# Optimization experiments

Hardware: AMD Instinct MI355X
Metric: run time of the kernel (lower is better)

The kernel has to match this reference:

```python
import jax, jax.numpy as jnp
import numpy as np

T = 22        # TypeEncoder.tensor_size() (assumed)
H = 2         # attention heads
C = 64        # hc_graph (per-head out channels)
L = 3         # num_hops
LEAFCAT = 5   # len(LeafType.valid_categories()) (assumed)
NSIZES = 8    # len(LeafType.valid_sizes()) (assumed)
HL = 64       # hc_linear
HT = 64       # hc_task == hc_leafsize
SLOPE = 0.2   # PyG GATConv negative_slope


def _gat(x, src, dst, W, asrc, adst, b):
    # PyG GATConv (concat=True, dropout=0, self-loops already appended to src/dst)
    N = x.shape[0]
    h = (x @ W).reshape(N, H, C)                      # [N,H,C]
    a_s = jnp.einsum('nhc,hc->nh', h, asrc)            # per-node src score
    a_d = jnp.einsum('nhc,hc->nh', h, adst)            # per-node dst score
    e = jax.nn.leaky_relu(a_s[src] + a_d[dst], SLOPE)  # [E+N,H]
    m = jax.ops.segment_max(e, dst, num_segments=N)
    p = jnp.exp(e - m[dst])
    s = jax.ops.segment_sum(p, dst, num_segments=N)
    alpha = p / (s[dst] + 1e-16)                       # scatter-softmax over in-edges
    out = jax.ops.segment_sum(h[src] * alpha[:, :, None], dst, num_segments=N)
    return out.reshape(N, H * C) + b


def _mlp2(z, W1, b1, W2, b2):
    return jax.nn.relu(z @ W1 + b1) @ W2 + b2


def setup_inputs() -> dict:
    key = jax.random.key(0)
    ks = jax.random.split(key, 32)
    N, E, NG, NPG = 102400, 1228800, 256, 400
    D = H * C
    g = lambda k, shp, fan: (jax.random.normal(k, shp, jnp.float32) / np.sqrt(fan)).astype(jnp.float32)
    z = lambda *shp: jnp.zeros(shp, jnp.float32)
    return {
        'x': jax.random.normal(ks[0], (N, D), jnp.float32),
        'edge_index': jax.random.randint(ks[1], (2, E), 0, N),
        'batch': jnp.repeat(jnp.arange(NG, dtype=jnp.int32), NPG),
        'gat_W': g(ks[2], (L, D, D), D),
        'gat_asrc': g(ks[3], (L, H, C), C),
        'gat_adst': g(ks[4], (L, H, C), C),
        'gat_b': z(L, D),
        'shared_W': g(ks[5], (D + T, HL), D + T),
        'shared_b': z(HL),
        'ptr_W1': g(ks[6], (3, HL, HT), HL), 'ptr_b1': z(3, HT),
        'ptr_W2': g(ks[7], (3, HT, 3), HT), 'ptr_b2': z(3, 3),
        'cat_W1': g(ks[8], (HL, HT), HL), 'cat_b1': z(HT),
        'cat_W2': g(ks[9], (HT, LEAFCAT), HT), 'cat_b2': z(LEAFCAT),
        'sf_W1': g(ks[10], (2, HL, HT), HL), 'sf_b1': z(2, HT),
        'sf_W2': g(ks[11], (2, HT, 1), HT), 'sf_b2': z(2, 1),
        'bool_W1': g(ks[12], (HL + T + LEAFCAT + 2, HT), HL + T + LEAFCAT + 2), 'bool_b1': z(HT),
        'bool_W2': g(ks[13], (HT, 1), HT), 'bool_b2': z(1),
        'size_W1': g(ks[14], (HL + T + LEAFCAT + 3, HT), HL + T + LEAFCAT + 3), 'size_b1': z(HT),
        'size_W2': g(ks[15], (HT, NSIZES), HT), 'size_b2': z(NSIZES),
    }


def reference(x, edge_index, batch, gat_W, gat_asrc, gat_adst, gat_b,
              shared_W, shared_b, ptr_W1, ptr_b1, ptr_W2, ptr_b2,
              cat_W1, cat_b1, cat_W2, cat_b2, sf_W1, sf_b1, sf_W2, sf_b2,
              bool_W1, bool_b1, bool_W2, bool_b2, size_W1, size_b1, size_W2, size_b2):
    N = x.shape[0]
    num_graphs = int(batch[-1]) + 1                    # batch is sorted per-graph ids
    node0 = jnp.searchsorted(batch, jnp.arange(num_graphs))  # first node of each graph
    dtype_vec = x[node0, :T]                           # NodeEncoder.split_node_vec dtype slice
    loops = jnp.arange(N)
    src = jnp.concatenate([edge_index[0], loops])      # GATConv add_self_loops=True
    dst = jnp.concatenate([edge_index[1], loops])
    h = x
    for l in range(L):
        h = _gat(h, src, dst, gat_W[l], gat_asrc[l], gat_adst[l], gat_b[l])
        if l < L - 1:
            h = jax.nn.relu(h)
    zf = jax.nn.relu(jnp.concatenate([h[node0], dtype_vec], axis=1) @ shared_W + shared_b)
    # 3 pointer heads, batched
    p = jax.nn.relu(jnp.einsum('gh,khd->kgd', zf, ptr_W1) + ptr_b1[:, None, :])
    ptr = jnp.einsum('kgd,kdo->kgo', p, ptr_W2) + ptr_b2[:, None, :]
    cat_logits = _mlp2(zf, cat_W1, cat_b1, cat_W2, cat_b2)
    q = jax.nn.relu(jnp.einsum('gh,khd->kgd', zf, sf_W1) + sf_b1[:, None, :])
    sf = jnp.einsum('kgd,kdo->kgo', q, sf_W2) + sf_b2[:, None, :]
    signed, floating = sf[0], sf[1]
    bool_in = jnp.concatenate([zf, dtype_vec, cat_logits, signed, floating], axis=1)
    bool_logit = _mlp2(bool_in, bool_W1, bool_b1, bool_W2, bool_b2)
    size_in = jnp.concatenate([bool_in, bool_logit], axis=1)
    size_logits = _mlp2(size_in, size_W1, size_b1, size_W2, size_b2)
    return (ptr[0], ptr[1], ptr[2], cat_logits, signed, floating, bool_logit, size_logits)
```

## Files before the change

kernel.cpp:

```cpp
#include <hip/hip_runtime.h>
#include <hip/hip_bf16.h>

typedef __hip_bfloat16 bf16;
typedef __attribute__((ext_vector_type(8))) short short8;
typedef __attribute__((ext_vector_type(4))) float floatx4;

#define MF(a, b, c) __builtin_amdgcn_mfma_f32_16x16x32_bf16(a, b, c, 0, 0, 0)

__device__ __forceinline__ float b2f(bf16 v) { return __bfloat162float(v); }
__device__ __forceinline__ unsigned short f2us(float f) {
    bf16 h = __float2bfloat16(f);
    return *(unsigned short*)&h;
}
__device__ __forceinline__ float lo2f(unsigned hv) { return __uint_as_float(hv << 16); }
__device__ __forceinline__ float hi2f(unsigned hv) { return __uint_as_float(hv & 0xffff0000u); }
__device__ __forceinline__ float leaky(float v) { return v > 0.f ? v : 0.2f * v; }

__device__ __forceinline__ float ldw(const void* p, size_t i, int f32) {
    return f32 ? ((const float*)p)[i] : b2f(((const bf16*)p)[i]);
}

template <int F32>
__device__ __forceinline__ float LDWt(const void* p, size_t i) {
    return F32 ? ((const float*)p)[i] : b2f(((const bf16*)p)[i]);
}

__device__ __forceinline__ int or16(const int* f) {
    int r = 0;
#pragma unroll
    for (int j = 0; j < 16; j++) r |= f[j];
    return r;
}

__device__ __forceinline__ void quadred(float part[4]) {
#pragma unroll
    for (int m = 1; m <= 8; m <<= 1)
#pragma unroll
        for (int r = 0; r < 4; r++) part[r] += __shfl_xor(part[r], m);
}

__global__ void k_detect_zero(const void* x, int* flagv, char* zbase, size_t zbytes,
                              const int* __restrict__ batch, int* __restrict__ node0,
                              unsigned char* __restrict__ rootb,
                              unsigned char* __restrict__ flag2, int N, int zBlocks) {
    int b = blockIdx.x;
    int t = threadIdx.x;
    if (b < 16) {
        __shared__ int sbad;
        if (t == 0) sbad = 0;
        __syncthreads();
        float v = b2f(((const bf16*)x)[b * 256 + t]);
        if (!(fabsf(v) < 1e10f)) sbad = 1;
        __syncthreads();
        if (t == 0) flagv[b] = sbad;
    } else if (b < 16 + zBlocks) {
        size_t off = (size_t)(b - 16) * 4096 + (size_t)t * 16;
        if (off < zbytes) *(uint4*)(zbase + off) = make_uint4(0u, 0u, 0u, 0u);
    } else {
        int i = (b - 16 - zBlocks) * 256 + t;
        if (i < N) {
            int bb = batch[i];
            int isroot = (i == 0) || (batch[i - 1] != bb);
            rootb[i] = (unsigned char)isroot;
            flag2[i] = (unsigned char)isroot;
            if (isroot) node0[bb] = i;
        }
    }
}

__global__ void k_prep_fused(const void* __restrict__ x, unsigned short* __restrict__ Ab,
                             int nvec,
                             const void* __restrict__ gw, unsigned short* __restrict__ Wt,
                             const void* as_, const void* ad_, const void* b_,
                             float* asF, float* adF, float* bF,
                             const void* sW_, const void* pW1_, const void* cW1_,
                             const void* fW1_, const void* bW1_, const void* zW1_,
                             unsigned short* __restrict__ Whd,
                             const int* __restrict__ ei, const unsigned char* __restrict__ rootb,
                             unsigned char* __restrict__ flag2, int E,
                             const int* __restrict__ flagv, int nbx8) {
    int b = blockIdx.x;
    int t = threadIdx.x;
    int f32 = or16(flagv);
    if (b < nbx8) {
        if (!f32) return;
        int i = b * 256 + t;
        if (i < nvec) {
            float4 a = ((const float4*)x)[2 * i];
            float4 c = ((const float4*)x)[2 * i + 1];
            uint4 o;
            o.x = ((unsigned)f2us(a.y) << 16) | f2us(a.x);
            o.y = ((unsigned)f2us(a.w) << 16) | f2us(a.z);
            o.z = ((unsigned)f2us(c.y) << 16) | f2us(c.x);
            o.w = ((unsigned)f2us(c.w) << 16) | f2us(c.z);
            ((uint4*)Ab)[i] = o;
        }
    } else if (b < nbx8 + 192) {
        int i = (b - nbx8) * 256 + t;
        int l = i >> 14, rem = i & 16383, n = rem >> 7, k = rem & 127;
        Wt[i] = f2us(ldw(gw, (size_t)l * 16384 + (size_t)k * 128 + n, f32));
    } else if (b < nbx8 + 194) {
        int i = (b - nbx8 - 192) * 256 + t;
        if (i < 384) {
            asF[i] = ldw(as_, i, f32);
            adF[i] = ldw(ad_, i, f32);
            bF[i] = ldw(b_, i, f32);
        }
    } else if (b < nbx8 + 194 + 184) {
        int i = (b - nbx8 - 194) * 256 + t;
        float v;
        if (i < 10240) {
            int n = i / 160, k = i - n * 160;
            v = (k < 150) ? ldw(sW_, (size_t)k * 64 + n, f32) : 0.f;
        } else if (i < 22528) {
            int j = i - 10240;
            int kk = j >> 12, r = j & 4095, n = r >> 6, k = r & 63;
            v = ldw(pW1_, (size_t)kk * 4096 + (size_t)k * 64 + n, f32);
        } else if (i < 26624) {
            int j = i - 22528;
            int n = j >> 6, k = j & 63;
            v = ldw(cW1_, (size_t)k * 64 + n, f32);
        } else if (i < 34816) {
            int j = i - 26624;
            int kk = j >> 12, r = j & 4095, n = r >> 6, k = r & 63;
            v = ldw(fW1_, (size_t)kk * 4096 + (size_t)k * 64 + n, f32);
        } else if (i < 40960) {
            int j = i - 34816;
            int n = j / 96, k = j - n * 96;
            v = (k < 93) ? ldw(bW1_, (size_t)k * 64 + n, f32) : 0.f;
        } else {
            int j = i - 40960;
            int n = j / 96, k = j - n * 96;
            v = (k < 94) ? ldw(zW1_, (size_t)k * 64 + n, f32) : 0.f;
        }
        Whd[i] = f2us(v);
    } else {
        int e = (b - nbx8 - 194 - 184) * 256 + t;
        if (e < E && rootb[ei[E + e]]) flag2[ei[e]] = 1;
    }
}

__global__ void k_hist_masked(const int* __restrict__ ei, const unsigned char* __restrict__ flag1,
                              int* __restrict__ counts, int E) {
    int e = blockIdx.x * blockDim.x + threadIdx.x;
    if (e < E) {
        int d = ei[E + e];
        if (flag1[d]) atomicAdd(&counts[d], 1);
    }
}

__global__ void k_scan3x(const int* __restrict__ counts,
                         const unsigned char* __restrict__ flag1,
                         const unsigned char* __restrict__ flag2,
                         int* __restrict__ offs, int* __restrict__ wp1, int* __restrict__ wp2,
                         int* __restrict__ bsums, int n) {
    __shared__ int s[256];
    int tid = threadIdx.x;
    int i = blockIdx.x * 256 + tid;
#pragma unroll
    for (int a = 0; a < 3; a++) {
        int v = 0;
        if (i < n) v = (a == 0) ? counts[i] : (a == 1) ? (int)flag1[i] : (int)flag2[i];
        s[tid] = v;
        __syncthreads();
        for (int d = 1; d < 256; d <<= 1) {
            int t2 = (tid >= d) ? s[tid - d] : 0;
            __syncthreads();
            s[tid] += t2;
            __syncthreads();
        }
        int incl = s[tid];
        if (i < n) {
            if (a == 0) offs[i] = incl - v;
            else if (a == 1) wp1[i] = incl - v;
            else wp2[i] = incl - v;
        }
        if (tid == 255) bsums[a * 512 + blockIdx.x] = incl;
        __syncthreads();
    }
}

__global__ void k_scan2x(int* __restrict__ bsums, int nb, int* __restrict__ nact) {
    __shared__ int s[512];
    int tid = threadIdx.x;
#pragma unroll
    for (int a = 0; a < 3; a++) {
        int* arr = bsums + a * 512;
        int v = (tid < nb) ? arr[tid] : 0;
        s[tid] = v;
        __syncthreads();
        for (int d = 1; d < 512; d <<= 1) {
            int t2 = (tid >= d) ? s[tid - d] : 0;
            __syncthreads();
            s[tid] += t2;
            __syncthreads();
        }
        arr[tid] = s[tid] - v;
        if (a >= 1 && tid == 511) nact[a - 1] = s[511];
        __syncthreads();
    }
}

__global__ void k_scatter_wl(const int* __restrict__ ei, const int* __restrict__ offs,
                             const int* __restrict__ bsums, int* __restrict__ cur,
                             const unsigned char* __restrict__ flag1,
                             const unsigned char* __restrict__ flag2,
                             const int* __restrict__ wp1, const int* __restrict__ wp2,
                             int* __restrict__ adj, int* __restrict__ wl1, int* __restrict__ wl2,
                             int E, int N, int eBlocks) {
    int b = blockIdx.x;
    if (b < eBlocks) {
        int e = b * 256 + threadIdx.x;
        if (e >= E) return;
        int d = ei[E + e];
        if (!flag1[d]) return;
        int r = atomicAdd(&cur[d], 1);
        adj[offs[d] + bsums[d >> 8] + r] = ei[e];
    } else {
        int i = (b - eBlocks) * 256 + threadIdx.x;
        if (i < N) {
            if (flag1[i]) wl1[wp1[i] + bsums[512 + (i >> 8)]] = i;
            if (flag2[i]) wl2[wp2[i] + bsums[1024 + (i >> 8)]] = i;
        }
    }
}

__device__ __forceinline__ void gemm_body(
    const unsigned short* __restrict__ Asrc, const unsigned short* __restrict__ Wt,
    unsigned short* __restrict__ Bb, float4* __restrict__ asadv,
    const float* __restrict__ asF, const float* __restrict__ adF, int N,
    const int* __restrict__ wl, const int* __restrict__ nactp, int bb) {
    __shared__ __align__(16) unsigned short Ws[128 * 136];
    __shared__ __align__(16) unsigned short Cs[64 * 136];

    int t = threadIdx.x;
    int r0 = bb * 64;
    int nact = wl ? *nactp : N;
    if (r0 >= nact) return;

    {
        const uint4* src = (const uint4*)Wt;
#pragma unroll
        for (int k = 0; k < 8; k++) {
            int j = t + k * 256;
            int row = j >> 4, c16 = j & 15;
            *(uint4*)&Ws[row * 136 + c16 * 8] = src[j];
        }
    }
    __syncthreads();

    int lane = t & 63;
    int w = t >> 6;
    int ln = lane & 15;
    int quad = lane >> 4;

    int idx = r0 + w * 16 + ln;
    bool valid = idx < nact;
    int arow = idx < N ? idx : N - 1;
    if (wl) arow = valid ? wl[idx] : 0;
    bool wave_active = __any((int)valid);

    if (wave_active) {
        const unsigned short* ap = Asrc + (size_t)arow * 128 + quad * 8;

        short8 afrag[4];
        if (valid) {
#pragma unroll
            for (int kt = 0; kt < 4; kt++)
                afrag[kt] = *(const short8*)(ap + kt * 32);
        } else {
#pragma unroll
            for (int kt = 0; kt < 4; kt++)
                afrag[kt] = (short8){0, 0, 0, 0, 0, 0, 0, 0};
        }

        floatx4 acc[8];
#pragma unroll
        for (int nt = 0; nt < 8; nt++) acc[nt] = (floatx4){0.f, 0.f, 0.f, 0.f};

#pragma unroll
        for (int nt = 0; nt < 8; nt++) {
            const unsigned short* wp = Ws + (nt * 16 + ln) * 136 + quad * 8;
#pragma unroll
            for (int kt = 0; kt < 4; kt++) {
                short8 bfrag = *(const short8*)(wp + kt * 32);
                acc[nt] = MF(afrag[kt], bfrag, acc[nt]);
            }
        }

        float as0[4] = {0, 0, 0, 0}, as1[4] = {0, 0, 0, 0};
        float ad0[4] = {0, 0, 0, 0}, ad1[4] = {0, 0, 0, 0};
#pragma unroll
        for (int nt = 0; nt < 8; nt++) {
            float asc = asF[nt * 16 + ln];
            float adc = adF[nt * 16 + ln];
#pragma unroll
            for (int r = 0; r < 4; r++) {
                float v = acc[nt][r];
                Cs[(w * 16 + quad * 4 + r) * 136 + nt * 16 + ln] = f2us(v);
                if (nt < 4) { as0[r] += v * asc; ad0[r] += v * adc; }
                else        { as1[r] += v * asc; ad1[r] += v * adc; }
            }
        }
#pragma unroll
        for (int mask = 1; mask <= 8; mask <<= 1) {
#pragma unroll
            for (int r = 0; r < 4; r++) {
                as0[r] += __shfl_xor(as0[r], mask);
                as1[r] += __shfl_xor(as1[r], mask);
                ad0[r] += __shfl_xor(ad0[r], mask);
                ad1[r] += __shfl_xor(ad1[r], mask);
            }
        }
        if (ln == 0) {
#pragma unroll
            for (int r = 0; r < 4; r++) {
                int idx3 = r0 + w * 16 + quad * 4 + r;
                if (idx3 < nact) {
                    int row = wl ? wl[idx3] : idx3;
                    asadv[row] = make_float4(as0[r], as1[r], ad0[r], ad1[r]);
                }
            }
        }
    }
    __syncthreads();

    {
        int idx2 = r0 + (t >> 2);
        int cseg = (t & 3) * 32;
        if (idx2 < nact) {
            int grow = wl ? wl[idx2] : idx2;
            const short8* srcp = (const short8*)&Cs[(t >> 2) * 136 + cseg];
            short8* dstp = (short8*)&Bb[(size_t)grow * 128 + cseg];
#pragma unroll
            for (int u = 0; u < 4; u++) dstp[u] = srcp[u];
        }
    }
}

__global__ __launch_bounds__(256) void k_gemm_mfma(
    const unsigned short* __restrict__ Ab, const unsigned short* __restrict__ Wt,
    unsigned short* __restrict__ Bb, float4* __restrict__ asadv,
    const float* __restrict__ asF, const float* __restrict__ adF, int N,
    const int* __restrict__ wl, const int* __restrict__ nactp) {
    gemm_body(Ab, Wt, Bb, asadv, asF, adF, N, wl, nactp, blockIdx.x);
}

__global__ __launch_bounds__(256) void k_gemm0_mark(
    const unsigned short* __restrict__ Ab, const void* __restrict__ xraw,
    const unsigned short* __restrict__ Wt,
    unsigned short* __restrict__ Bb, float4* __restrict__ asadv,
    const float* __restrict__ asF, const float* __restrict__ adF, int N,
    const int* __restrict__ ei, const unsigned char* __restrict__ flag2,
    unsigned char* __restrict__ flag1, int E, int markE, int markN,
    const int* __restrict__ flagv) {
    int b = blockIdx.x;
    if (b < markE) {
        int e = b * 256 + threadIdx.x;
        if (e < E && flag2[ei[E + e]]) flag1[ei[e]] = 1;
        return;
    }
    if (b < markE + markN) {
        int i = (b - markE) * 256 + threadIdx.x;
        if (i < N && flag2[i]) flag1[i] = 1;
        return;
    }
    const unsigned short* Asrc = or16(flagv) ? Ab : (const unsigned short*)xraw;
    gemm_body(Asrc, Wt, Bb, asadv, asF, adF, N, nullptr, nullptr, b - markE - markN);
}

__global__ void k_gat_agg(const uint2* __restrict__ Bu2, const float4* __restrict__ asadv,
                          const int* __restrict__ offs, const int* __restrict__ bsums,
                          const int* __restrict__ counts,
                          const int* __restrict__ adj, const float* __restrict__ biasF,
                          uint2* __restrict__ Au2, float2* __restrict__ pE,
                          const int* __restrict__ nactp, int nfix, int dorelu, int byidx,
                          const int* __restrict__ wl) {
    int wave = (blockIdx.x * blockDim.x + threadIdx.x) >> 6;
    int lane = threadIdx.x & 63;
    int hl = lane & 31;
    int hb = lane & 32;
    int idx = wave * 2 + (lane >> 5);
    int n = nfix ? nfix : *nactp;
    if (idx >= n) return;
    int node = wl[idx];
    int head = hl >> 4;

    float4 self = asadv[node];
    float ad0 = self.z, ad1 = self.w;
    float es0 = __expf(leaky(self.x + ad0));
    float es1 = __expf(leaky(self.y + ad1));

    int o = offs[node] + bsums[node >> 8];
    int c = counts[node];
    uint2 hvs = Bu2[(size_t)node * 32 + hl];
    float acc0, acc1, acc2, acc3;

    if (c <= 32) {
        int src_r = 0;
        float p0 = 0.f, p1 = 0.f;
        if (hl < c) {
            src_r = adj[o + hl];
            float4 av = asadv[src_r];
            p0 = __expf(leaky(av.x + ad0));
            p1 = __expf(leaky(av.y + ad1));
        }
        float t0 = p0, t1 = p1;
#pragma unroll
        for (int mask = 1; mask <= 16; mask <<= 1) {
            t0 += __shfl_xor(t0, mask);
            t1 += __shfl_xor(t1, mask);
        }
        float inv0 = 1.f / (es0 + t0 + 1e-16f);
        float inv1 = 1.f / (es1 + t1 + 1e-16f);
        p0 *= inv0;
        p1 *= inv1;
        float aself = head ? es1 * inv1 : es0 * inv0;
        acc0 = aself * lo2f(hvs.x);
        acc1 = aself * hi2f(hvs.x);
        acc2 = aself * lo2f(hvs.y);
        acc3 = aself * hi2f(hvs.y);

        uint2 hq[4];
#pragma unroll
        for (int j = 0; j < 4; j++) {
            int s2 = __shfl(src_r, hb + j);
            hq[j] = make_uint2(0u, 0u);
            if (j < c) hq[j] = Bu2[(size_t)s2 * 32 + hl];
        }

        for (int base = 0; base < c; base += 4) {
            uint2 cu[4];
            float av4[4];
#pragma unroll
            for (int j = 0; j < 4; j++) {
                cu[j] = hq[j];
                int idx2 = (base + j) & 31;
                float a0 = __shfl(p0, hb + idx2);
                float a1 = __shfl(p1, hb + idx2);
                float a = head ? a1 : a0;
                av4[j] = (base + j < c) ? a : 0.f;
            }
#pragma unroll
            for (int j = 0; j < 4; j++) {
                int nx = base + 4 + j;
                int s2 = __shfl(src_r, hb + (nx & 31));
                if (nx < c) hq[j] = Bu2[(size_t)s2 * 32 + hl];
            }
#pragma unroll
            for (int j = 0; j < 4; j++) {
                acc0 += av4[j] * lo2f(cu[j].x);
                acc1 += av4[j] * hi2f(cu[j].x);
                acc2 += av4[j] * lo2f(cu[j].y);
                acc3 += av4[j] * hi2f(cu[j].y);
            }
        }
    } else {
        float sum0 = es0, sum1 = es1;
        for (int base = 0; base < c; base += 32) {
            int i = base + hl;
            float p0 = 0.f, p1 = 0.f;
            if (i < c) {
                int s = adj[o + i];
                float4 av = asadv[s];
                p0 = __expf(leaky(av.x + ad0));
                p1 = __expf(leaky(av.y + ad1));
                pE[o + i] = make_float2(p0, p1);
            }
            float t0 = p0, t1 = p1;
#pragma unroll
            for (int mask = 1; mask <= 16; mask <<= 1) {
                t0 += __shfl_xor(t0, mask);
                t1 += __shfl_xor(t1, mask);
            }
            sum0 += t0; sum1 += t1;
        }
        float inv0 = 1.f / (sum0 + 1e-16f);
        float inv1 = 1.f / (sum1 + 1e-16f);
        float aself = head ? es1 * inv1 : es0 * inv0;
        float invh = head ? inv1 : inv0;
        acc0 = aself * lo2f(hvs.x);
        acc1 = aself * hi2f(hvs.x);
        acc2 = aself * lo2f(hvs.y);
        acc3 = aself * hi2f(hvs.y);
        for (int i = 0; i < c; i++) {
            int s = adj[o + i];
            float2 pp = pE[o + i];
            uint2 hv = Bu2[(size_t)s * 32 + hl];
            float a = (head ? pp.y : pp.x) * invh;
            acc0 += a * lo2f(hv.x);
            acc1 += a * hi2f(hv.x);
            acc2 += a * lo2f(hv.y);
            acc3 += a * hi2f(hv.y);
        }
    }

    float4 bb4 = ((const float4*)biasF)[hl];
    float q0 = acc0 + bb4.x;
    float q1 = acc1 + bb4.y;
    float q2 = acc2 + bb4.z;
    float q3 = acc3 + bb4.w;
    if (dorelu) {
        q0 = fmaxf(q0, 0.f); q1 = fmaxf(q1, 0.f);
        q2 = fmaxf(q2, 0.f); q3 = fmaxf(q3, 0.f);
    }
    Au2[(size_t)(byidx ? idx : node) * 32 + hl] =
        make_uint2(((unsigned)f2us(q1) << 16) | f2us(q0),
                   ((unsigned)f2us(q3) << 16) | f2us(q2));
}

template <int F32>
__device__ void heads_mfma_body(
    const unsigned* __restrict__ hroot32, const void* __restrict__ x,
    const int* __restrict__ node0, const unsigned short* __restrict__ Whd,
    const void* sb, const void* pb1, const void* pW2, const void* pb2,
    const void* cb1, const void* cW2, const void* cb2,
    const void* fb1, const void* fW2, const void* fb2,
    const void* bb1, const void* bW2, const void* bb2,
    const void* zb1, const void* zW2, const void* zb2,
    void* __restrict__ outv) {
    __shared__ __align__(16) unsigned short hinS[64 * 168];
    __shared__ __align__(16) unsigned short TwS[4][16 * 168];

    int t = threadIdx.x;
    int g0b = blockIdx.x * 64;
    bf16* outb = (bf16*)outv;
    float* outf = (float*)outv;
#define STORE(idx, val) do { if (F32) outf[idx] = (val); else outb[idx] = __float2bfloat16(val); } while (0)

    {
        unsigned* h32 = (unsigned*)hinS;
        for (int j = t; j < 64 * 64; j += 256) {
            int gl = j >> 6, c = j & 63;
            h32[gl * 84 + c] = hroot32[(size_t)(g0b + gl) * 64 + c];
        }
        for (int j = t; j < 64 * 20; j += 256) {
            int gl = j / 20, c = j - gl * 20;
            int n0 = node0[g0b + gl];
            int k0 = 2 * c;
            float d0 = (k0 < 22) ? LDWt<F32>(x, (size_t)n0 * 128 + k0) : 0.f;
            float d1 = (k0 + 1 < 22) ? LDWt<F32>(x, (size_t)n0 * 128 + k0 + 1) : 0.f;
            h32[gl * 84 + 64 + c] = ((unsigned)f2us(d1) << 16) | f2us(d0);
        }
    }
    __syncthreads();

    int w = t >> 6;
    int lane = t & 63;
    int ln = lane & 15, quad = lane >> 4;
    unsigned short* T = TwS[w];
    int gq = quad * 4;
    int gw0 = g0b + w * 16;

    for (int j = lane; j < 16 * 32; j += 64) {
        int gl = j >> 5, c = j & 31;
        T[gl * 168 + 64 + c] =
            (c < 22) ? hinS[(w * 16 + gl) * 168 + 128 + c] : (unsigned short)0;
    }

    short8 afA[5];
#pragma unroll
    for (int kt = 0; kt < 5; kt++)
        afA[kt] = *(const short8*)&hinS[(w * 16 + ln) * 168 + quad * 8 + kt * 32];
#pragma unroll
    for (int nt = 0; nt < 4; nt++) {
        floatx4 acc = (floatx4){0.f, 0.f, 0.f, 0.f};
        const unsigned short* bp = Whd + (nt * 16 + ln) * 160 + quad * 8;
#pragma unroll
        for (int kt = 0; kt < 5; kt++)
            acc = MF(afA[kt], *(const short8*)(bp + kt * 32), acc);
        float bias = LDWt<F32>(sb, nt * 16 + ln);
#pragma unroll
        for (int r = 0; r < 4; r++)
            T[(gq + r) * 168 + nt * 16 + ln] = f2us(fmaxf(acc[r] + bias, 0.f));
    }
    __syncthreads();

    short8 af20 = *(const short8*)&T[ln * 168 + quad * 8];
    short8 af21 = *(const short8*)&T[ln * 168 + quad * 8 + 32];

#pragma unroll
    for (int k = 0; k < 3; k++) {
        const unsigned short* Bw = Whd + 10240 + k * 4096;
        floatx4 acc[4];
#pragma unroll
        for (int nt = 0; nt < 4; nt++) {
            floatx4 a = (floatx4){0.f, 0.f, 0.f, 0.f};
            const unsigned short* bp = Bw + (nt * 16 + ln) * 64 + quad * 8;
            a = MF(af20, *(const short8*)bp, a);
            a = MF(af21, *(const short8*)(bp + 32), a);
            float b1 = LDWt<F32>(pb1, k * 64 + nt * 16 + ln);
#pragma unroll
            for (int r = 0; r < 4; r++) a[r] = fmaxf(a[r] + b1, 0.f);
            acc[nt] = a;
        }
#pragma unroll
        for (int o = 0; o < 3; o++) {
            float w2[4], part[4];
#pragma unroll
            for (int nt = 0; nt < 4; nt++)
                w2[nt] = LDWt<F32>(pW2, (size_t)k * 192 + (size_t)(nt * 16 + ln) * 3 + o);
#pragma unroll
            for (int r = 0; r < 4; r++)
                part[r] = acc[0][r] * w2[0] + acc[1][r] * w2[1] +
                          acc[2][r] * w2[2] + acc[3][r] * w2[3];
            quadred(part);
            if (ln == 0) {
                float b2 = LDWt<F32>(pb2, k * 3 + o);
#pragma unroll
                for (int r = 0; r < 4; r++)
                    STORE(k * 768 + (gw0 + gq + r) * 3 + o, part[r] + b2);
            }
        }
    }

    {
        const unsigned short* Bw = Whd + 22528;
        floatx4 acc[4];
#pragma unroll
        for (int nt = 0; nt < 4; nt++) {
            floatx4 a = (floatx4){0.f, 0.f, 0.f, 0.f};
            const unsigned short* bp = Bw + (nt * 16 + ln) * 64 + quad * 8;
            a = MF(af20, *(const short8*)bp, a);
            a = MF(af21, *(const short8*)(bp + 32), a);
            float b1 = LDWt<F32>(cb1, nt * 16 + ln);
#pragma unroll
            for (int r = 0; r < 4; r++) a[r] = fmaxf(a[r] + b1, 0.f);
            acc[nt] = a;
        }
#pragma unroll
        for (int o = 0; o < 5; o++) {
            float w2[4], part[4];
#pragma unroll
            for (int nt = 0; nt < 4; nt++)
                w2[nt] = LDWt<F32>(cW2, (size_t)(nt * 16 + ln) * 5 + o);
#pragma unroll
            for (int r = 0; r < 4; r++)
                part[r] = acc[0][r] * w2[0] + acc[1][r] * w2[1] +
                          acc[2][r] * w2[2] + acc[3][r] * w2[3];
            quadred(part);
            if (ln == 0) {
                float b2 = LDWt<F32>(cb2, o);
#pragma unroll
                for (int r = 0; r < 4; r++) {
                    float v = part[r] + b2;
                    T[(gq + r) * 168 + 86 + o] = f2us(v);
                    STORE(2304 + (gw0 + gq + r) * 5 + o, v);
                }
            }
        }
    }

#pragma unroll
    for (int k = 0; k < 2; k++) {
        const unsigned short* Bw = Whd + 26624 + k * 4096;
        floatx4 acc[4];
#pragma unroll
        for (int nt = 0; nt < 4; nt++) {
            floatx4 a = (floatx4){0.f, 0.f, 0.f, 0.f};
            const unsigned short* bp = Bw + (nt * 16 + ln) * 64 + quad * 8;
            a = MF(af20, *(const short8*)bp, a);
            a = MF(af21, *(const short8*)(bp + 32), a);
            float b1 = LDWt<F32>(fb1, k * 64 + nt * 16 + ln);
#pragma unroll
            for (int r = 0; r < 4; r++) a[r] = fmaxf(a[r] + b1, 0.f);
            acc[nt] = a;
        }
        float w2[4], part[4];
#pragma unroll
        for (int nt = 0; nt < 4; nt++)
            w2[nt] = LDWt<F32>(fW2, (size_t)k * 64 + nt * 16 + ln);
#pragma unroll
        for (int r = 0; r < 4; r++)
            part[r] = acc[0][r] * w2[0] + acc[1][r] * w2[1] +
                      acc[2][r] * w2[2] + acc[3][r] * w2[3];
        quadred(part);
        if (ln == 0) {
            float b2 = LDWt<F32>(fb2, k);
#pragma unroll
            for (int r = 0; r < 4; r++) {
                float v = part[r] + b2;
                T[(gq + r) * 168 + 91 + k] = f2us(v);
                STORE(3584 + k * 256 + (gw0 + gq + r), v);
            }
        }
    }
    __syncthreads();

    short8 af3 = *(const short8*)&T[ln * 168 + 64 + quad * 8];

    {
        const unsigned short* Bw = Whd + 34816;
        floatx4 acc[4];
#pragma unroll
        for (int nt = 0; nt < 4; nt++) {
            floatx4 a = (floatx4){0.f, 0.f, 0.f, 0.f};
            const unsigned short* bp = Bw + (nt * 16 + ln) * 96 + quad * 8;
            a = MF(af20, *(const short8*)bp, a);
            a = MF(af21, *(const short8*)(bp + 32), a);
            a = MF(af3, *(const short8*)(bp + 64), a);
            float b1 = LDWt<F32>(bb1, nt * 16 + ln);
#pragma unroll
            for (int r = 0; r < 4; r++) a[r] = fmaxf(a[r] + b1, 0.f);
            acc[nt] = a;
        }
        float w2[4], part[4];
#pragma unroll
        for (int nt = 0; nt < 4; nt++)
            w2[nt] = LDWt<F32>(bW2, nt * 16 + ln);
#pragma unroll
        for (int r = 0; r < 4; r++)
            part[r] = acc[0][r] * w2[0] + acc[1][r] * w2[1] +
                      acc[2][r] * w2[2] + acc[3][r] * w2[3];
        quadred(part);
        if (ln == 0) {
            float b2 = LDWt<F32>(bb2, 0);
#pragma unroll
            for (int r = 0; r < 4; r++) {
                float v = part[r] + b2;
                T[(gq + r) * 168 + 93] = f2us(v);
                STORE(4096 + (gw0 + gq + r), v);
            }
        }
    }
    __syncthreads();

    af3 = *(const short8*)&T[ln * 168 + 64 + quad * 8];

    {
        const unsigned short* Bw = Whd + 40960;
        floatx4 acc[4];
#pragma unroll
        for (int nt = 0; nt < 4; nt++) {
            floatx4 a = (floatx4){0.f, 0.f, 0.f, 0.f};
            const unsigned short* bp = Bw + (nt * 16 + ln) * 96 + quad * 8;
            a = MF(af20, *(const short8*)bp, a);
            a = MF(af21, *(const short8*)(bp + 32), a);
            a = MF(af3, *(const short8*)(bp + 64), a);
            float b1 = LDWt<F32>(zb1, nt * 16 + ln);
#pragma unroll
            for (int r = 0; r < 4; r++) a[r] = fmaxf(a[r] + b1, 0.f);
            acc[nt] = a;
        }
#pragma unroll
        for (int o = 0; o < 8; o++) {
            float w2[4], part[4];
#pragma unroll
            for (int nt = 0; nt < 4; nt++)
                w2[nt] = LDWt<F32>(zW2, (size_t)(nt * 16 + ln) * 8 + o);
#pragma unroll
            for (int r = 0; r < 4; r++)
                part[r] = acc[0][r] * w2[0] + acc[1][r] * w2[1] +
                          acc[2][r] * w2[2] + acc[3][r] * w2[3];
            quadred(part);
            if (ln == 0) {
                float b2 = LDWt<F32>(zb2, o);
#pragma unroll
                for (int r = 0; r < 4; r++)
                    STORE(4352 + (gw0 + gq + r) * 8 + o, part[r] + b2);
            }
        }
    }
#undef STORE
}

__global__ __launch_bounds__(256) void k_heads_mfma(
    const unsigned* __restrict__ hroot32, const void* __restrict__ x,
    const int* __restrict__ node0, const unsigned short* __restrict__ Whd,
    const void* sb, const void* pb1, const void* pW2, const void* pb2,
    const void* cb1, const void* cW2, const void* cb2,
    const void* fb1, const void* fW2, const void* fb2,
    const void* bb1, const void* bW2, const void* bb2,
    const void* zb1, const void* zW2, const void* zb2,
    void* __restrict__ outv, const int* __restrict__ flagv) {
    if (or16(flagv))
        heads_mfma_body<1>(hroot32, x, node0, Whd, sb, pb1, pW2, pb2, cb1, cW2, cb2,
                           fb1, fW2, fb2, bb1, bW2, bb2, zb1, zW2, zb2, outv);
    else
        heads_mfma_body<0>(hroot32, x, node0, Whd, sb, pb1, pW2, pb2, cb1, cW2, cb2,
                           fb1, fW2, fb2, bb1, bW2, bb2, zb1, zW2, zb2, outv);
}


extern "C" void kernel_launch(void* const* d_in, const int* in_sizes, int n_in,
                              void* d_out, int out_size, void* d_ws, size_t ws_size,
                              hipStream_t stream) {
    const void* x     = d_in[0];
    const int*  ei    = (const int*)d_in[1];
    const int*  batch = (const int*)d_in[2];

    int N = in_sizes[0] / 128;
    int E = in_sizes[1] / 2;

    char* w = (char*)d_ws;
    float4* asad = (float4*)w;              w += (size_t)N * 16;
    unsigned short* A = (unsigned short*)w; w += (size_t)N * 128 * 2;
    unsigned short* B = (unsigned short*)w; w += (size_t)N * 128 * 2;
    float2* pE = (float2*)w;                w += (size_t)E * 8;
    unsigned short* Wt = (unsigned short*)w; w += 3 * 16384 * 2;
    unsigned short* Whd = (unsigned short*)w; w += 47104 * 2;
    float* asF = (float*)w;                 w += 384 * 4;
    float* adF = (float*)w;                 w += 384 * 4;
    float* bF = (float*)w;                  w += 384 * 4;
    int* offs = (int*)w;                    w += (size_t)N * 4;
    int* wp1 = (int*)w;                     w += (size_t)N * 4;
    int* wp2 = (int*)w;                     w += (size_t)N * 4;
    int* wl1 = (int*)w;                     w += (size_t)N * 4;
    int* wl2 = (int*)w;                     w += (size_t)N * 4;
    int* adj = (int*)w;                     w += (size_t)E * 4;
    int* bsums = (int*)w;                   w += 3 * 512 * 4;
    int* node0 = (int*)w;                   w += 256 * 4;
    int* nact = (int*)w;                    w += 64;
    unsigned* hroot = (unsigned*)w;         w += 256 * 128 * 2;
    char* zbase = w;
    int* counts = (int*)w;                  w += (size_t)N * 4;
    int* cur = (int*)w;                     w += (size_t)N * 4;
    unsigned char* flag1 = (unsigned char*)w; w += (size_t)N;
    size_t zbytes = (size_t)N * 9;
    int* flagv = (int*)w;                   w += 64;
    unsigned char* rootb = (unsigned char*)w; w += (size_t)N;
    unsigned char* flag2 = (unsigned char*)w; w += (size_t)N;

    int nb = (N + 255) / 256;
    int nvec = N * 16;
    int nbx8 = (nvec + 255) / 256;
    int nbE = (E + 255) / 256;
    int gemmBlocks = (N + 63) / 64;
    int zBlocks = (int)((zbytes + 4095) / 4096);

    k_detect_zero<<<16 + zBlocks + nb, 256, 0, stream>>>(
        x, flagv, zbase, zbytes, batch, node0, rootb, flag2, N, zBlocks);

    k_prep_fused<<<nbx8 + 194 + 184 + nbE, 256, 0, stream>>>(
        x, A, nvec, d_in[3], Wt, d_in[4], d_in[5], d_in[6],
        asF, adF, bF,
        d_in[7], d_in[9], d_in[13], d_in[17], d_in[21], d_in[25], Whd,
        ei, rootb, flag2, E, flagv, nbx8);

    k_gemm0_mark<<<nbE + nb + gemmBlocks, 256, 0, stream>>>(
        A, x, Wt, B, asad, asF, adF, N, ei, flag2, flag1, E, nbE, nb, flagv);

    k_hist_masked<<<nbE, 256, 0, stream>>>(ei, flag1, counts, E);
    k_scan3x<<<nb, 256, 0, stream>>>(counts, flag1, flag2, offs, wp1, wp2, bsums, N);
    k_scan2x<<<1, 512, 0, stream>>>(bsums, nb, nact);
    k_scatter_wl<<<nbE + nb, 256, 0, stream>>>(
        ei, offs, bsums, cur, flag1, flag2, wp1, wp2, adj, wl1, wl2, E, N, nbE);

    int nwaves = (N + 1) / 2;
    int aggblocks = (nwaves + 3) / 4;

    k_gat_agg<<<aggblocks, 256, 0, stream>>>(
        (const uint2*)B, asad, offs, bsums, counts, adj, bF, (uint2*)A, pE,
        nact, 0, 1, 0, wl1);

    k_gemm_mfma<<<gemmBlocks, 256, 0, stream>>>(
        A, Wt + 16384, B, asad, asF + 128, adF + 128, N, wl1, nact);
    k_gat_agg<<<aggblocks, 256, 0, stream>>>(
        (const uint2*)B, asad, offs, bsums, counts, adj, bF + 128, (uint2*)A, pE,
        nact + 1, 0, 1, 0, wl2);

    k_gemm_mfma<<<gemmBlocks, 256, 0, stream>>>(
        A, Wt + 2 * 16384, B, asad, asF + 256, adF + 256, N, wl2, nact + 1);

    k_gat_agg<<<32, 256, 0, stream>>>(
        (const uint2*)B, asad, offs, bsums, counts, adj, bF + 256, (uint2*)hroot, pE,
        nact, 256, 0, 1, node0);

    k_heads_mfma<<<4, 256, 0, stream>>>(
        hroot, x, node0, Whd,
        d_in[8], d_in[10], d_in[11], d_in[12],
        d_in[14], d_in[15], d_in[16],
        d_in[18], d_in[19], d_in[20],
        d_in[22], d_in[23], d_in[24],
        d_in[26], d_in[27], d_in[28],
        d_out, flagv);
}
```

Baseline: 316.3 us.

## Replace CSR adjacency with fixed-slot buckets and drop the count/scan passes

Incoming edges are now scattered into a fixed per-node array of 128 slots, with an overflow list for larger degrees. This removes the histogram kernel, the count scan and the offset computation. The two remaining flag scans and the block-sum scan are merged into one kernel that uses a last-block-done atomic. The GEMM and aggregation kernels become grid-stride loops with smaller fixed grids, and the root-flag/dtype-detect setup is simplified. The cost is a much larger adjacency buffer (N*128 ints) with scattered memory access, plus a linear scan of the overflow list for any node above 128 in-edges.

```diff
diff --git a/kernel.cpp b/kernel.cpp
--- a/kernel.cpp
+++ b/kernel.cpp
@@ -6,6 +6,7 @@
 typedef __attribute__((ext_vector_type(4))) float floatx4;
 
 #define MF(a, b, c) __builtin_amdgcn_mfma_f32_16x16x32_bf16(a, b, c, 0, 0, 0)
+#define ADJ_SLOTS 128
 
 __device__ __forceinline__ float b2f(bf16 v) { return __bfloat162float(v); }
 __device__ __forceinline__ unsigned short f2us(float f) {
@@ -25,13 +26,6 @@
     return F32 ? ((const float*)p)[i] : b2f(((const bf16*)p)[i]);
 }
 
-__device__ __forceinline__ int or16(const int* f) {
-    int r = 0;
-#pragma unroll
-    for (int j = 0; j < 16; j++) r |= f[j];
-    return r;
-}
-
 __device__ __forceinline__ void quadred(float part[4]) {
 #pragma unroll
     for (int m = 1; m <= 8; m <<= 1)
@@ -39,75 +33,75 @@
         for (int r = 0; r < 4; r++) part[r] += __shfl_xor(part[r], m);
 }
 
-__global__ void k_detect_zero(const void* x, int* flagv, char* zbase, size_t zbytes,
+__global__ void k_detect_zero(const void* x, int* flagd, char* zbase, size_t zbytes,
                               const int* __restrict__ batch, int* __restrict__ node0,
-                              unsigned char* __restrict__ rootb,
                               unsigned char* __restrict__ flag2, int N, int zBlocks) {
     int b = blockIdx.x;
     int t = threadIdx.x;
-    if (b < 16) {
+    if (b == 0) {
         __shared__ int sbad;
         if (t == 0) sbad = 0;
         __syncthreads();
-        float v = b2f(((const bf16*)x)[b * 256 + t]);
-        if (!(fabsf(v) < 1e10f)) sbad = 1;
+        const bf16* xb = (const bf16*)x;
+        int bad = 0;
+#pragma unroll
+        for (int j = 0; j < 16; j++) {
+            float v = b2f(xb[t * 16 + j]);
+            if (!(fabsf(v) < 1e10f)) bad = 1;
+        }
+        if (bad) sbad = 1;
         __syncthreads();
-        if (t == 0) flagv[b] = sbad;
-    } else if (b < 16 + zBlocks) {
-        size_t off = (size_t)(b - 16) * 4096 + (size_t)t * 16;
+        if (t == 0) flagd[0] = sbad;
+    } else if (b < 1 + zBlocks) {
+        size_t off = (size_t)(b - 1) * 4096 + (size_t)t * 16;
         if (off < zbytes) *(uint4*)(zbase + off) = make_uint4(0u, 0u, 0u, 0u);
     } else {
-        int i = (b - 16 - zBlocks) * 256 + t;
+        int i = (b - 1 - zBlocks) * 256 + t;
         if (i < N) {
             int bb = batch[i];
             int isroot = (i == 0) || (batch[i - 1] != bb);
-            rootb[i] = (unsigned char)isroot;
             flag2[i] = (unsigned char)isroot;
             if (isroot) node0[bb] = i;
         }
     }
 }
 
-__global__ void k_prep_fused(const void* __restrict__ x, unsigned short* __restrict__ Ab,
-                             int nvec,
-                             const void* __restrict__ gw, unsigned short* __restrict__ Wt,
-                             const void* as_, const void* ad_, const void* b_,
-                             float* asF, float* adF, float* bF,
-                             const void* sW_, const void* pW1_, const void* cW1_,
-                             const void* fW1_, const void* bW1_, const void* zW1_,
-                             unsigned short* __restrict__ Whd,
-                             const int* __restrict__ ei, const unsigned char* __restrict__ rootb,
-                             unsigned char* __restrict__ flag2, int E,
-                             const int* __restrict__ flagv, int nbx8) {
+__global__ void k_prep(const void* __restrict__ x, unsigned short* __restrict__ Ab,
+                       int nvec,
+                       const void* __restrict__ gw, unsigned short* __restrict__ Wt,
+                       const void* as_, const void* ad_, const void* b_,
+                       float* asF, float* adF, float* bF,
+                       const void* sW_, const void* pW1_, const void* cW1_,
+                       const void* fW1_, const void* bW1_, const void* zW1_,
+                       unsigned short* __restrict__ Whd,
+                       const int* __restrict__ ei, const int* __restrict__ batch,
+                       unsigned char* __restrict__ flag2, int E,
+                       const int* __restrict__ flagd, int nbE) {
     int b = blockIdx.x;
     int t = threadIdx.x;
-    int f32 = or16(flagv);
-    if (b < nbx8) {
-        if (!f32) return;
+    if (b < nbE) {
+        int e = b * 256 + t;
+        if (e < E) {
+            int d = ei[E + e];
+            if (d == 0 || batch[d] != batch[d - 1]) flag2[ei[e]] = 1;
+        }
+        return;
+    }
+    int f32 = *flagd;
+    b -= nbE;
+    if (b < 192) {
         int i = b * 256 + t;
-        if (i < nvec) {
-            float4 a = ((const float4*)x)[2 * i];
-            float4 c = ((const float4*)x)[2 * i + 1];
-            uint4 o;
-            o.x = ((unsigned)f2us(a.y) << 16) | f2us(a.x);
-            o.y = ((unsigned)f2us(a.w) << 16) | f2us(a.z);
-            o.z = ((unsigned)f2us(c.y) << 16) | f2us(c.x);
-            o.w = ((unsigned)f2us(c.w) << 16) | f2us(c.z);
-            ((uint4*)Ab)[i] = o;
-        }
-    } else if (b < nbx8 + 192) {
-        int i = (b - nbx8) * 256 + t;
         int l = i >> 14, rem = i & 16383, n = rem >> 7, k = rem & 127;
         Wt[i] = f2us(ldw(gw, (size_t)l * 16384 + (size_t)k * 128 + n, f32));
-    } else if (b < nbx8 + 194) {
-        int i = (b - nbx8 - 192) * 256 + t;
+    } else if (b < 194) {
+        int i = (b - 192) * 256 + t;
         if (i < 384) {
             asF[i] = ldw(as_, i, f32);
             adF[i] = ldw(ad_, i, f32);
             bF[i] = ldw(b_, i, f32);
         }
-    } else if (b < nbx8 + 194 + 184) {
-        int i = (b - nbx8 - 194) * 256 + t;
+    } else if (b < 194 + 184) {
+        int i = (b - 194) * 256 + t;
         float v;
         if (i < 10240) {
             int n = i / 160, k = i - n * 160;
@@ -135,32 +129,35 @@
         }
         Whd[i] = f2us(v);
     } else {
-        int e = (b - nbx8 - 194 - 184) * 256 + t;
-        if (e < E && rootb[ei[E + e]]) flag2[ei[e]] = 1;
-    }
-}
-
-__global__ void k_hist_masked(const int* __restrict__ ei, const unsigned char* __restrict__ flag1,
-                              int* __restrict__ counts, int E) {
-    int e = blockIdx.x * blockDim.x + threadIdx.x;
-    if (e < E) {
-        int d = ei[E + e];
-        if (flag1[d]) atomicAdd(&counts[d], 1);
-    }
-}
-
-__global__ void k_scan3x(const int* __restrict__ counts,
-                         const unsigned char* __restrict__ flag1,
-                         const unsigned char* __restrict__ flag2,
-                         int* __restrict__ offs, int* __restrict__ wp1, int* __restrict__ wp2,
-                         int* __restrict__ bsums, int n) {
+        if (!f32) return;
+        int i0 = (b - 194 - 184) * 256 + t;
+        for (int i = i0; i < nvec; i += 256 * 256) {
+            float4 a = ((const float4*)x)[2 * i];
+            float4 c = ((const float4*)x)[2 * i + 1];
+            uint4 o;
+            o.x = ((unsigned)f2us(a.y) << 16) | f2us(a.x);
+            o.y = ((unsigned)f2us(a.w) << 16) | f2us(a.z);
+            o.z = ((unsigned)f2us(c.y) << 16) | f2us(c.x);
+            o.w = ((unsigned)f2us(c.w) << 16) | f2us(c.z);
+            ((uint4*)Ab)[i] = o;
+        }
+    }
+}
+
+__global__ void k_scan2lane(const unsigned char* __restrict__ flag1,
+                            const unsigned char* __restrict__ flag2,
+                            int* __restrict__ wp1, int* __restrict__ wp2,
+                            int* __restrict__ bsums, int* __restrict__ nact,
+                            int* __restrict__ done, int n, int nb) {
     __shared__ int s[256];
+    __shared__ int s2[512];
+    __shared__ int lastFlag;
     int tid = threadIdx.x;
     int i = blockIdx.x * 256 + tid;
 #pragma unroll
-    for (int a = 0; a < 3; a++) {
+    for (int a = 0; a < 2; a++) {
         int v = 0;
-        if (i < n) v = (a == 0) ? counts[i] : (a == 1) ? (int)flag1[i] : (int)flag2[i];
+        if (i < n) v = a == 0 ? (int)flag1[i] : (int)flag2[i];
         s[tid] = v;
         __syncthreads();
         for (int d = 1; d < 256; d <<= 1) {
@@ -171,42 +168,50 @@
         }
         int incl = s[tid];
         if (i < n) {
-            if (a == 0) offs[i] = incl - v;
-            else if (a == 1) wp1[i] = incl - v;
+            if (a == 0) wp1[i] = incl - v;
             else wp2[i] = incl - v;
         }
         if (tid == 255) bsums[a * 512 + blockIdx.x] = incl;
         __syncthreads();
     }
-}
-
-__global__ void k_scan2x(int* __restrict__ bsums, int nb, int* __restrict__ nact) {
-    __shared__ int s[512];
-    int tid = threadIdx.x;
-#pragma unroll
-    for (int a = 0; a < 3; a++) {
+    __threadfence();
+    if (tid == 0) lastFlag = (atomicAdd(done, 1) == nb - 1);
+    __syncthreads();
+    if (!lastFlag) return;
+    __threadfence();
+#pragma unroll
+    for (int a = 0; a < 2; a++) {
         int* arr = bsums + a * 512;
-        int v = (tid < nb) ? arr[tid] : 0;
-        s[tid] = v;
+        int v0 = (tid < nb) ? arr[tid] : 0;
+        int v1 = (tid + 256 < nb) ? arr[tid + 256] : 0;
+        s2[tid] = v0;
+        s2[tid + 256] = v1;
         __syncthreads();
         for (int d = 1; d < 512; d <<= 1) {
-            int t2 = (tid >= d) ? s[tid - d] : 0;
+            int a0 = (tid >= d) ? s2[tid - d] : 0;
+            int a1 = (tid + 256 >= d) ? s2[tid + 256 - d] : 0;
             __syncthreads();
-            s[tid] += t2;
+            s2[tid] += a0;
+            s2[tid + 256] += a1;
             __syncthreads();
         }
-        arr[tid] = s[tid] - v;
-        if (a >= 1 && tid == 511) nact[a - 1] = s[511];
+        arr[tid] = s2[tid] - v0;
+        arr[tid + 256] = s2[tid + 256] - v1;
+        if (tid == 255) nact[a] = s2[511];
         __syncthreads();
     }
 }
 
-__global__ void k_scatter_wl(const int* __restrict__ ei, const int* __restrict__ offs,
-                             const int* __restrict__ bsums, int* __restrict__ cur,
+__global__ void k_scatter_wl(const int* __restrict__ ei,
+                             int* __restrict__ cur,
                              const unsigned char* __restrict__ flag1,
                              const unsigned char* __restrict__ flag2,
                              const int* __restrict__ wp1, const int* __restrict__ wp2,
-                             int* __restrict__ adj, int* __restrict__ wl1, int* __restrict__ wl2,
+                             const int* __restrict__ bsums,
+                             int* __restrict__ adj,
+                             int* __restrict__ ovfD, int* __restrict__ ovfS,
+                             int* __restrict__ ovfCnt,
+                             int* __restrict__ wl1, int* __restrict__ wl2,
                              int E, int N, int eBlocks) {
     int b = blockIdx.x;
     if (b < eBlocks) {
@@ -214,13 +219,18 @@
         if (e >= E) return;
         int d = ei[E + e];
         if (!flag1[d]) return;
-        int r = atomicAdd(&cur[d], 1);
-        adj[offs[d] + bsums[d >> 8] + r] = ei[e];
+        int slot = atomicAdd(&cur[d], 1);
+        if (slot < ADJ_SLOTS) {
+            adj[(size_t)d * ADJ_SLOTS + slot] = ei[e];
+        } else {
+            int o = atomicAdd(ovfCnt, 1);
+            if (o < E) { ovfD[o] = d; ovfS[o] = ei[e]; }
+        }
     } else {
         int i = (b - eBlocks) * 256 + threadIdx.x;
         if (i < N) {
-            if (flag1[i]) wl1[wp1[i] + bsums[512 + (i >> 8)]] = i;
-            if (flag2[i]) wl2[wp2[i] + bsums[1024 + (i >> 8)]] = i;
+            if (flag1[i]) wl1[wp1[i] + bsums[i >> 8]] = i;
+            if (flag2[i]) wl2[wp2[i] + bsums[512 + (i >> 8)]] = i;
         }
     }
 }
@@ -229,14 +239,14 @@
     const unsigned short* __restrict__ Asrc, const unsigned short* __restrict__ Wt,
     unsigned short* __restrict__ Bb, float4* __restrict__ asadv,
     const float* __restrict__ asF, const float* __restrict__ adF, int N,
-    const int* __restrict__ wl, const int* __restrict__ nactp, int bb) {
+    const int* __restrict__ wl, const int* __restrict__ nactp,
+    int bb0, int bstride) {
     __shared__ __align__(16) unsigned short Ws[128 * 136];
     __shared__ __align__(16) unsigned short Cs[64 * 136];
 
     int t = threadIdx.x;
-    int r0 = bb * 64;
     int nact = wl ? *nactp : N;
-    if (r0 >= nact) return;
+    if (bb0 * 64 >= nact) return;
 
     {
         const uint4* src = (const uint4*)Wt;
@@ -254,87 +264,91 @@
     int ln = lane & 15;
     int quad = lane >> 4;
 
-    int idx = r0 + w * 16 + ln;
-    bool valid = idx < nact;
-    int arow = idx < N ? idx : N - 1;
-    if (wl) arow = valid ? wl[idx] : 0;
-    bool wave_active = __any((int)valid);
-
-    if (wave_active) {
-        const unsigned short* ap = Asrc + (size_t)arow * 128 + quad * 8;
-
-        short8 afrag[4];
-        if (valid) {
-#pragma unroll
-            for (int kt = 0; kt < 4; kt++)
-                afrag[kt] = *(const short8*)(ap + kt * 32);
-        } else {
-#pragma unroll
-            for (int kt = 0; kt < 4; kt++)
-                afrag[kt] = (short8){0, 0, 0, 0, 0, 0, 0, 0};
-        }
-
-        floatx4 acc[8];
-#pragma unroll
-        for (int nt = 0; nt < 8; nt++) acc[nt] = (floatx4){0.f, 0.f, 0.f, 0.f};
-
-#pragma unroll
-        for (int nt = 0; nt < 8; nt++) {
-            const unsigned short* wp = Ws + (nt * 16 + ln) * 136 + quad * 8;
-#pragma unroll
-            for (int kt = 0; kt < 4; kt++) {
-                short8 bfrag = *(const short8*)(wp + kt * 32);
-                acc[nt] = MF(afrag[kt], bfrag, acc[nt]);
-            }
-        }
-
-        float as0[4] = {0, 0, 0, 0}, as1[4] = {0, 0, 0, 0};
-        float ad0[4] = {0, 0, 0, 0}, ad1[4] = {0, 0, 0, 0};
-#pragma unroll
-        for (int nt = 0; nt < 8; nt++) {
-            float asc = asF[nt * 16 + ln];
-            float adc = adF[nt * 16 + ln];
-#pragma unroll
-            for (int r = 0; r < 4; r++) {
-                float v = acc[nt][r];
-                Cs[(w * 16 + quad * 4 + r) * 136 + nt * 16 + ln] = f2us(v);
-                if (nt < 4) { as0[r] += v * asc; ad0[r] += v * adc; }
-                else        { as1[r] += v * asc; ad1[r] += v * adc; }
-            }
-        }
-#pragma unroll
-        for (int mask = 1; mask <= 8; mask <<= 1) {
-#pragma unroll
-            for (int r = 0; r < 4; r++) {
-                as0[r] += __shfl_xor(as0[r], mask);
-                as1[r] += __shfl_xor(as1[r], mask);
-                ad0[r] += __shfl_xor(ad0[r], mask);
-                ad1[r] += __shfl_xor(ad1[r], mask);
-            }
-        }
-        if (ln == 0) {
-#pragma unroll
-            for (int r = 0; r < 4; r++) {
-                int idx3 = r0 + w * 16 + quad * 4 + r;
-                if (idx3 < nact) {
-                    int row = wl ? wl[idx3] : idx3;
-                    asadv[row] = make_float4(as0[r], as1[r], ad0[r], ad1[r]);
-                }
-            }
-        }
-    }
-    __syncthreads();
-
-    {
-        int idx2 = r0 + (t >> 2);
-        int cseg = (t & 3) * 32;
-        if (idx2 < nact) {
-            int grow = wl ? wl[idx2] : idx2;
-            const short8* srcp = (const short8*)&Cs[(t >> 2) * 136 + cseg];
-            short8* dstp = (short8*)&Bb[(size_t)grow * 128 + cseg];
-#pragma unroll
-            for (int u = 0; u < 4; u++) dstp[u] = srcp[u];
-        }
+    for (int bb = bb0; bb * 64 < nact; bb += bstride) {
+        int r0 = bb * 64;
+        int idx = r0 + w * 16 + ln;
+        bool valid = idx < nact;
+        int arow = idx < N ? idx : N - 1;
+        if (wl) arow = valid ? wl[idx] : 0;
+        bool wave_active = __any((int)valid);
+
+        if (wave_active) {
+            const unsigned short* ap = Asrc + (size_t)arow * 128 + quad * 8;
+
+            short8 afrag[4];
+            if (valid) {
+#pragma unroll
+                for (int kt = 0; kt < 4; kt++)
+                    afrag[kt] = *(const short8*)(ap + kt * 32);
+            } else {
+#pragma unroll
+                for (int kt = 0; kt < 4; kt++)
+                    afrag[kt] = (short8){0, 0, 0, 0, 0, 0, 0, 0};
+            }
+
+            floatx4 acc[8];
+#pragma unroll
+            for (int nt = 0; nt < 8; nt++) acc[nt] = (floatx4){0.f, 0.f, 0.f, 0.f};
+
+#pragma unroll
+            for (int nt = 0; nt < 8; nt++) {
+                const unsigned short* wp = Ws + (nt * 16 + ln) * 136 + quad * 8;
+#pragma unroll
+                for (int kt = 0; kt < 4; kt++) {
+                    short8 bfrag = *(const short8*)(wp + kt * 32);
+                    acc[nt] = MF(afrag[kt], bfrag, acc[nt]);
+                }
+            }
+
+            float as0[4] = {0, 0, 0, 0}, as1[4] = {0, 0, 0, 0};
+            float ad0[4] = {0, 0, 0, 0}, ad1[4] = {0, 0, 0, 0};
+#pragma unroll
+            for (int nt = 0; nt < 8; nt++) {
+                float asc = asF[nt * 16 + ln];
+                float adc = adF[nt * 16 + ln];
+#pragma unroll
+                for (int r = 0; r < 4; r++) {
+                    float v = acc[nt][r];
+                    Cs[(w * 16 + quad * 4 + r) * 136 + nt * 16 + ln] = f2us(v);
+                    if (nt < 4) { as0[r] += v * asc; ad0[r] += v * adc; }
+                    else        { as1[r] += v * asc; ad1[r] += v * adc; }
+                }
+            }
+#pragma unroll
+            for (int mask = 1; mask <= 8; mask <<= 1) {
+#pragma unroll
+                for (int r = 0; r < 4; r++) {
+                    as0[r] += __shfl_xor(as0[r], mask);
+                    as1[r] += __shfl_xor(as1[r], mask);
+                    ad0[r] += __shfl_xor(ad0[r], mask);
+                    ad1[r] += __shfl_xor(ad1[r], mask);
+                }
+            }
+            if (ln == 0) {
+#pragma unroll
+                for (int r = 0; r < 4; r++) {
+                    int idx3 = r0 + w * 16 + quad * 4 + r;
+                    if (idx3 < nact) {
+                        int row = wl ? wl[idx3] : idx3;
+                        asadv[row] = make_float4(as0[r], as1[r], ad0[r], ad1[r]);
+                    }
+                }
+            }
+        }
+        __syncthreads();
+
+        {
+            int idx2 = r0 + (t >> 2);
+            int cseg = (t & 3) * 32;
+            if (idx2 < nact) {
+                int grow = wl ? wl[idx2] : idx2;
+                const short8* srcp = (const short8*)&Cs[(t >> 2) * 136 + cseg];
+                short8* dstp = (short8*)&Bb[(size_t)grow * 128 + cseg];
+#pragma unroll
+                for (int u = 0; u < 4; u++) dstp[u] = srcp[u];
+            }
+        }
+        __syncthreads();
     }
 }
 
@@ -343,7 +357,7 @@
     unsigned short* __restrict__ Bb, float4* __restrict__ asadv,
     const float* __restrict__ asF, const float* __restrict__ adF, int N,
     const int* __restrict__ wl, const int* __restrict__ nactp) {
-    gemm_body(Ab, Wt, Bb, asadv, asF, adF, N, wl, nactp, blockIdx.x);
+    gemm_body(Ab, Wt, Bb, asadv, asF, adF, N, wl, nactp, blockIdx.x, gridDim.x);
 }
 
 __global__ __launch_bounds__(256) void k_gemm0_mark(
@@ -353,7 +367,7 @@
     const float* __restrict__ asF, const float* __restrict__ adF, int N,
     const int* __restrict__ ei, const unsigned char* __restrict__ flag2,
     unsigned char* __restrict__ flag1, int E, int markE, int markN,
-    const int* __restrict__ flagv) {
+    const int* __restrict__ flagd) {
     int b = blockIdx.x;
     if (b < markE) {
         int e = b * 256 + threadIdx.x;
@@ -365,107 +379,51 @@
         if (i < N && flag2[i]) flag1[i] = 1;
         return;
     }
-    const unsigned short* Asrc = or16(flagv) ? Ab : (const unsigned short*)xraw;
-    gemm_body(Asrc, Wt, Bb, asadv, asF, adF, N, nullptr, nullptr, b - markE - markN);
+    const unsigned short* Asrc = *flagd ? Ab : (const unsigned short*)xraw;
+    gemm_body(Asrc, Wt, Bb, asadv, asF, adF, N, nullptr, nullptr,
+              b - markE - markN, gridDim.x - markE - markN);
 }
 
 __global__ void k_gat_agg(const uint2* __restrict__ Bu2, const float4* __restrict__ asadv,
-                          const int* __restrict__ offs, const int* __restrict__ bsums,
-                          const int* __restrict__ counts,
-                          const int* __restrict__ adj, const float* __restrict__ biasF,
-                          uint2* __restrict__ Au2, float2* __restrict__ pE,
+                          const int* __restrict__ cur, const int* __restrict__ adj,
+                          const int* __restrict__ ovfD, const int* __restrict__ ovfS,
+                          const int* __restrict__ ovfCnt,
+                          const float* __restrict__ biasF,
+                          uint2* __restrict__ Au2,
                           const int* __restrict__ nactp, int nfix, int dorelu, int byidx,
                           const int* __restrict__ wl) {
-    int wave = (blockIdx.x * blockDim.x + threadIdx.x) >> 6;
+    int totWaves = (gridDim.x * blockDim.x) >> 6;
+    int wave0 = (blockIdx.x * blockDim.x + threadIdx.x) >> 6;
     int lane = threadIdx.x & 63;
     int hl = lane & 31;
     int hb = lane & 32;
-    int idx = wave * 2 + (lane >> 5);
+    int half = lane >> 5;
+    int head = hl >> 4;
     int n = nfix ? nfix : *nactp;
-    if (idx >= n) return;
-    int node = wl[idx];
-    int head = hl >> 4;
-
-    float4 self = asadv[node];
-    float ad0 = self.z, ad1 = self.w;
-    float es0 = __expf(leaky(self.x + ad0));
-    float es1 = __expf(leaky(self.y + ad1));
-
-    int o = offs[node] + bsums[node >> 8];
-    int c = counts[node];
-    uint2 hvs = Bu2[(size_t)node * 32 + hl];
-    float acc0, acc1, acc2, acc3;
-
-    if (c <= 32) {
-        int src_r = 0;
-        float p0 = 0.f, p1 = 0.f;
-        if (hl < c) {
-            src_r = adj[o + hl];
-            float4 av = asadv[src_r];
-            p0 = __expf(leaky(av.x + ad0));
-            p1 = __expf(leaky(av.y + ad1));
-        }
-        float t0 = p0, t1 = p1;
-#pragma unroll
-        for (int mask = 1; mask <= 16; mask <<= 1) {
-            t0 += __shfl_xor(t0, mask);
-            t1 += __shfl_xor(t1, mask);
-        }
-        float inv0 = 1.f / (es0 + t0 + 1e-16f);
-        float inv1 = 1.f / (es1 + t1 + 1e-16f);
-        p0 *= inv0;
-        p1 *= inv1;
-        float aself = head ? es1 * inv1 : es0 * inv0;
-        acc0 = aself * lo2f(hvs.x);
-        acc1 = aself * hi2f(hvs.x);
-        acc2 = aself * lo2f(hvs.y);
-        acc3 = aself * hi2f(hvs.y);
-
-        uint2 hq[4];
-#pragma unroll
-        for (int j = 0; j < 4; j++) {
-            int s2 = __shfl(src_r, hb + j);
-            hq[j] = make_uint2(0u, 0u);
-            if (j < c) hq[j] = Bu2[(size_t)s2 * 32 + hl];
-        }
-
-        for (int base = 0; base < c; base += 4) {
-            uint2 cu[4];
-            float av4[4];
-#pragma unroll
-            for (int j = 0; j < 4; j++) {
-                cu[j] = hq[j];
-                int idx2 = (base + j) & 31;
-                float a0 = __shfl(p0, hb + idx2);
-                float a1 = __shfl(p1, hb + idx2);
-                float a = head ? a1 : a0;
-                av4[j] = (base + j < c) ? a : 0.f;
-            }
-#pragma unroll
-            for (int j = 0; j < 4; j++) {
-                int nx = base + 4 + j;
-                int s2 = __shfl(src_r, hb + (nx & 31));
-                if (nx < c) hq[j] = Bu2[(size_t)s2 * 32 + hl];
-            }
-#pragma unroll
-            for (int j = 0; j < 4; j++) {
-                acc0 += av4[j] * lo2f(cu[j].x);
-                acc1 += av4[j] * hi2f(cu[j].x);
-                acc2 += av4[j] * lo2f(cu[j].y);
-                acc3 += av4[j] * hi2f(cu[j].y);
-            }
-        }
-    } else {
-        float sum0 = es0, sum1 = es1;
-        for (int base = 0; base < c; base += 32) {
-            int i = base + hl;
+
+    for (int wv = wave0; wv * 2 < n; wv += totWaves) {
+        int idx = wv * 2 + half;
+        if (idx >= n) continue;
+        int node = wl[idx];
+
+        float4 self = asadv[node];
+        float ad0 = self.z, ad1 = self.w;
+        float es0 = __expf(leaky(self.x + ad0));
+        float es1 = __expf(leaky(self.y + ad1));
+
+        const int* ap = adj + (size_t)node * ADJ_SLOTS;
+        int c = cur[node];
+        uint2 hvs = Bu2[(size_t)node * 32 + hl];
+        float acc0, acc1, acc2, acc3;
+
+        if (c <= 32) {
+            int src_r = 0;
             float p0 = 0.f, p1 = 0.f;
-            if (i < c) {
-                int s = adj[o + i];
-                float4 av = asadv[s];
+            if (hl < c) {
+                src_r = ap[hl];
+                float4 av = asadv[src_r];
                 p0 = __expf(leaky(av.x + ad0));
                 p1 = __expf(leaky(av.y + ad1));
-                pE[o + i] = make_float2(p0, p1);
             }
             float t0 = p0, t1 = p1;
 #pragma unroll
@@ -473,40 +431,123 @@
                 t0 += __shfl_xor(t0, mask);
                 t1 += __shfl_xor(t1, mask);
             }
-            sum0 += t0; sum1 += t1;
-        }
-        float inv0 = 1.f / (sum0 + 1e-16f);
-        float inv1 = 1.f / (sum1 + 1e-16f);
-        float aself = head ? es1 * inv1 : es0 * inv0;
-        float invh = head ? inv1 : inv0;
-        acc0 = aself * lo2f(hvs.x);
-        acc1 = aself * hi2f(hvs.x);
-        acc2 = aself * lo2f(hvs.y);
-        acc3 = aself * hi2f(hvs.y);
-        for (int i = 0; i < c; i++) {
-            int s = adj[o + i];
-            float2 pp = pE[o + i];
-            uint2 hv = Bu2[(size_t)s * 32 + hl];
-            float a = (head ? pp.y : pp.x) * invh;
-            acc0 += a * lo2f(hv.x);
-            acc1 += a * hi2f(hv.x);
-            acc2 += a * lo2f(hv.y);
-            acc3 += a * hi2f(hv.y);
-        }
-    }
-
-    float4 bb4 = ((const float4*)biasF)[hl];
-    float q0 = acc0 + bb4.x;
-    float q1 = acc1 + bb4.y;
-    float q2 = acc2 + bb4.z;
-    float q3 = acc3 + bb4.w;
-    if (dorelu) {
-        q0 = fmaxf(q0, 0.f); q1 = fmaxf(q1, 0.f);
-        q2 = fmaxf(q2, 0.f); q3 = fmaxf(q3, 0.f);
-    }
-    Au2[(size_t)(byidx ? idx : node) * 32 + hl] =
-        make_uint2(((unsigned)f2us(q1) << 16) | f2us(q0),
-                   ((unsigned)f2us(q3) << 16) | f2us(q2));
+            float inv0 = 1.f / (es0 + t0 + 1e-16f);
+            float inv1 = 1.f / (es1 + t1 + 1e-16f);
+            p0 *= inv0;
+            p1 *= inv1;
+            float aself = head ? es1 * inv1 : es0 * inv0;
+            acc0 = aself * lo2f(hvs.x);
+            acc1 = aself * hi2f(hvs.x);
+            acc2 = aself * lo2f(hvs.y);
+            acc3 = aself * hi2f(hvs.y);
+
+            uint2 hq[4];
+#pragma unroll
+            for (int j = 0; j < 4; j++) {
+                int s2 = __shfl(src_r, hb + j);
+                hq[j] = make_uint2(0u, 0u);
+                if (j < c) hq[j] = Bu2[(size_t)s2 * 32 + hl];
+            }
+
+            for (int base = 0; base < c; base += 4) {
+                uint2 cu[4];
+                float av4[4];
+#pragma unroll
+                for (int j = 0; j < 4; j++) {
+                    cu[j] = hq[j];
+                    int idx2 = (base + j) & 31;
+                    float a0 = __shfl(p0, hb + idx2);
+                    float a1 = __shfl(p1, hb + idx2);
+                    float a = head ? a1 : a0;
+                    av4[j] = (base + j < c) ? a : 0.f;
+                }
+#pragma unroll
+                for (int j = 0; j < 4; j++) {
+                    int nx = base + 4 + j;
+                    int s2 = __shfl(src_r, hb + (nx & 31));
+                    if (nx < c) hq[j] = Bu2[(size_t)s2 * 32 + hl];
+                }
+#pragma unroll
+                for (int j = 0; j < 4; j++) {
+                    acc0 += av4[j] * lo2f(cu[j].x);
+                    acc1 += av4[j] * hi2f(cu[j].x);
+                    acc2 += av4[j] * lo2f(cu[j].y);
+                    acc3 += av4[j] * hi2f(cu[j].y);
+                }
+            }
+        } else {
+            float sum0 = es0, sum1 = es1;
+            int cc = min(c, ADJ_SLOTS);
+            for (int base = 0; base < cc; base += 32) {
+                int i = base + hl;
+                float p0 = 0.f, p1 = 0.f;
+                if (i < cc) {
+                    int s = ap[i];
+                    float4 av = asadv[s];
+                    p0 = __expf(leaky(av.x + ad0));
+                    p1 = __expf(leaky(av.y + ad1));
+                }
+                float t0 = p0, t1 = p1;
+#pragma unroll
+                for (int mask = 1; mask <= 16; mask <<= 1) {
+                    t0 += __shfl_xor(t0, mask);
+                    t1 += __shfl_xor(t1, mask);
+                }
+                sum0 += t0; sum1 += t1;
+            }
+            int no = (c > ADJ_SLOTS) ? *ovfCnt : 0;
+            for (int oe = 0; oe < no; oe++) {
+                if (ovfD[oe] == node) {
+                    float4 av = asadv[ovfS[oe]];
+                    sum0 += __expf(leaky(av.x + ad0));
+                    sum1 += __expf(leaky(av.y + ad1));
+                }
+            }
+            float inv0 = 1.f / (sum0 + 1e-16f);
+            float inv1 = 1.f / (sum1 + 1e-16f);
+            float aself = head ? es1 * inv1 : es0 * inv0;
+            float invh = head ? inv1 : inv0;
+            acc0 = aself * lo2f(hvs.x);
+            acc1 = aself * hi2f(hvs.x);
+            acc2 = aself * lo2f(hvs.y);
+            acc3 = aself * hi2f(hvs.y);
+            for (int i = 0; i < cc; i++) {
+                int s = ap[i];
+                float4 av = asadv[s];
+                float a = (head ? __expf(leaky(av.y + ad1)) : __expf(leaky(av.x + ad0))) * invh;
+                uint2 hv = Bu2[(size_t)s * 32 + hl];
+                acc0 += a * lo2f(hv.x);
+                acc1 += a * hi2f(hv.x);
+                acc2 += a * lo2f(hv.y);
+                acc3 += a * hi2f(hv.y);
+            }
+            for (int oe = 0; oe < no; oe++) {
+                if (ovfD[oe] == node) {
+                    int s = ovfS[oe];
+                    float4 av = asadv[s];
+                    float a = (head ? __expf(leaky(av.y + ad1)) : __expf(leaky(av.x + ad0))) * invh;
+                    uint2 hv = Bu2[(size_t)s * 32 + hl];
+                    acc0 += a * lo2f(hv.x);
+                    acc1 += a * hi2f(hv.x);
+                    acc2 += a * lo2f(hv.y);
+                    acc3 += a * hi2f(hv.y);
+                }
+            }
+        }
+
+        float4 bb4 = ((const float4*)biasF)[hl];
+        float q0 = acc0 + bb4.x;
+        float q1 = acc1 + bb4.y;
+        float q2 = acc2 + bb4.z;
+        float q3 = acc3 + bb4.w;
+        if (dorelu) {
+            q0 = fmaxf(q0, 0.f); q1 = fmaxf(q1, 0.f);
+            q2 = fmaxf(q2, 0.f); q3 = fmaxf(q3, 0.f);
+        }
+        Au2[(size_t)(byidx ? idx : node) * 32 + hl] =
+            make_uint2(((unsigned)f2us(q1) << 16) | f2us(q0),
+                       ((unsigned)f2us(q3) << 16) | f2us(q2));
+    }
 }
 
 template <int F32>
@@ -772,8 +813,8 @@
     const void* fb1, const void* fW2, const void* fb2,
     const void* bb1, const void* bW2, const void* bb2,
     const void* zb1, const void* zW2, const void* zb2,
-    void* __restrict__ outv, const int* __restrict__ flagv) {
-    if (or16(flagv))
+    void* __restrict__ outv, const int* __restrict__ flagd) {
+    if (*flagd)
         heads_mfma_body<1>(hroot32, x, node0, Whd, sb, pb1, pW2, pb2, cb1, cW2, cb2,
                            fb1, fW2, fb2, bb1, bW2, bb2, zb1, zW2, zb2, outv);
     else
@@ -796,74 +837,70 @@
     float4* asad = (float4*)w;              w += (size_t)N * 16;
     unsigned short* A = (unsigned short*)w; w += (size_t)N * 128 * 2;
     unsigned short* B = (unsigned short*)w; w += (size_t)N * 128 * 2;
-    float2* pE = (float2*)w;                w += (size_t)E * 8;
     unsigned short* Wt = (unsigned short*)w; w += 3 * 16384 * 2;
     unsigned short* Whd = (unsigned short*)w; w += 47104 * 2;
     float* asF = (float*)w;                 w += 384 * 4;
     float* adF = (float*)w;                 w += 384 * 4;
     float* bF = (float*)w;                  w += 384 * 4;
-    int* offs = (int*)w;                    w += (size_t)N * 4;
     int* wp1 = (int*)w;                     w += (size_t)N * 4;
     int* wp2 = (int*)w;                     w += (size_t)N * 4;
     int* wl1 = (int*)w;                     w += (size_t)N * 4;
     int* wl2 = (int*)w;                     w += (size_t)N * 4;
-    int* adj = (int*)w;                     w += (size_t)E * 4;
+    int* adj = (int*)w;                     w += (size_t)N * ADJ_SLOTS * 4;
+    int* ovfD = (int*)w;                    w += (size_t)E * 4;
+    int* ovfS = (int*)w;                    w += (size_t)E * 4;
     int* bsums = (int*)w;                   w += 3 * 512 * 4;
     int* node0 = (int*)w;                   w += 256 * 4;
     int* nact = (int*)w;                    w += 64;
     unsigned* hroot = (unsigned*)w;         w += 256 * 128 * 2;
     char* zbase = w;
-    int* counts = (int*)w;                  w += (size_t)N * 4;
     int* cur = (int*)w;                     w += (size_t)N * 4;
     unsigned char* flag1 = (unsigned char*)w; w += (size_t)N;
-    size_t zbytes = (size_t)N * 9;
-    int* flagv = (int*)w;                   w += 64;
-    unsigned char* rootb = (unsigned char*)w; w += (size_t)N;
+    int* done = (int*)w;                    w += 64;
+    int* ovfCnt = (int*)w;                  w += 64;
+    size_t zbytes = (size_t)N * 5 + 128;
+    int* flagd = (int*)w;                   w += 64;
     unsigned char* flag2 = (unsigned char*)w; w += (size_t)N;
 
     int nb = (N + 255) / 256;
     int nvec = N * 16;
-    int nbx8 = (nvec + 255) / 256;
     int nbE = (E + 255) / 256;
-    int gemmBlocks = (N + 63) / 64;
     int zBlocks = (int)((zbytes + 4095) / 4096);
 
-    k_detect_zero<<<16 + zBlocks + nb, 256, 0, stream>>>(
-        x, flagv, zbase, zbytes, batch, node0, rootb, flag2, N, zBlocks);
-
-    k_prep_fused<<<nbx8 + 194 + 184 + nbE, 256, 0, stream>>>(
+    k_detect_zero<<<1 + zBlocks + nb, 256, 0, stream>>>(
+        x, flagd, zbase, zbytes, batch, node0, flag2, N, zBlocks);
+
+    k_prep<<<nbE + 194 + 184 + 256, 256, 0, stream>>>(
         x, A, nvec, d_in[3], Wt, d_in[4], d_in[5], d_in[6],
         asF, adF, bF,
         d_in[7], d_in[9], d_in[13], d_in[17], d_in[21], d_in[25], Whd,
-        ei, rootb, flag2, E, flagv, nbx8);
-
-    k_gemm0_mark<<<nbE + nb + gemmBlocks, 256, 0, stream>>>(
-        A, x, Wt, B, asad, asF, adF, N, ei, flag2, flag1, E, nbE, nb, flagv);
-
-    k_hist_masked<<<nbE, 256, 0, stream>>>(ei, flag1, counts, E);
-    k_scan3x<<<nb, 256, 0, stream>>>(counts, flag1, flag2, offs, wp1, wp2, bsums, N);
-    k_scan2x<<<1, 512, 0, stream>>>(bsums, nb, nact);
+        ei, batch, flag2, E, flagd, nbE);
+
+    k_gemm0_mark<<<nbE + nb + 800, 256, 0, stream>>>(
+        A, x, Wt, B, asad, asF, adF, N, ei, flag2, flag1, E, nbE, nb, flagd);
+
+    k_scan2lane<<<nb, 256, 0, stream>>>(flag1, flag2, wp1, wp2, bsums, nact, done, N, nb);
+
     k_scatter_wl<<<nbE + nb, 256, 0, stream>>>(
-        ei, offs, bsums, cur, flag1, flag2, wp1, wp2, adj, wl1, wl2, E, N, nbE);
-
-    int nwaves = (N + 1) / 2;
-    int aggblocks = (nwaves + 3) / 4;
-
-    k_gat_agg<<<aggblocks, 256, 0, stream>>>(
-        (const uint2*)B, asad, offs, bsums, counts, adj, bF, (uint2*)A, pE,
+        ei, cur, flag1, flag2, wp1, wp2, bsums, adj, ovfD, ovfS, ovfCnt,
+        wl1, wl2, E, N, nbE);
+
+    k_gat_agg<<<2048, 256, 0, stream>>>(
+        (const uint2*)B, asad, cur, adj, ovfD, ovfS, ovfCnt, bF, (uint2*)A,
         nact, 0, 1, 0, wl1);
 
-    k_gemm_mfma<<<gemmBlocks, 256, 0, stream>>>(
+    k_gemm_mfma<<<512, 256, 0, stream>>>(
         A, Wt + 16384, B, asad, asF + 128, adF + 128, N, wl1, nact);
-    k_gat_agg<<<aggblocks, 256, 0, stream>>>(
-        (const uint2*)B, asad, offs, bsums, counts, adj, bF + 128, (uint2*)A, pE,
+
+    k_gat_agg<<<512, 256, 0, stream>>>(
+        (const uint2*)B, asad, cur, adj, ovfD, ovfS, ovfCnt, bF + 128, (uint2*)A,
         nact + 1, 0, 1, 0, wl2);
 
-    k_gemm_mfma<<<gemmBlocks, 256, 0, stream>>>(
+    k_gemm_mfma<<<128, 256, 0, stream>>>(
         A, Wt + 2 * 16384, B, asad, asF + 256, adF + 256, N, wl2, nact + 1);
 
     k_gat_agg<<<32, 256, 0, stream>>>(
-        (const uint2*)B, asad, offs, bsums, counts, adj, bF + 256, (uint2*)hroot, pE,
+        (const uint2*)B, asad, cur, adj, ovfD, ovfS, ovfCnt, bF + 256, (uint2*)hroot,
         nact, 256, 0, 1, node0);
 
     k_heads_mfma<<<4, 256, 0, stream>>>(
@@ -873,5 +910,5 @@
         d_in[18], d_in[19], d_in[20],
         d_in[22], d_in[23], d_in[24],
         d_in[26], d_in[27], d_in[28],
-        d_out, flagv);
-}
+        d_out, flagd);
+}
```

Result: slower. 335.2 us (+6.0%).
